# Performance work log

Hardware: AMD Instinct MI355X
Metric: run time of the kernel (lower is better)

Reference implementation:

```python
import jax, jax.numpy as jnp
import numpy as np

B, S, D, H = 2, 2048, 1024, 16
HD = D // H  # head dim 64
LN_EPS = 1e-12


def setup_inputs() -> dict:
    key = jax.random.key(0)
    ks = jax.random.split(key, 10)
    sc = 0.02
    return {
        "input_tensor": jax.random.normal(ks[0], (B, S, D), dtype=jnp.float32),
        "attention_mask": jnp.zeros((B, 1, 1, S), dtype=jnp.float32),
        "Wq": jax.random.normal(ks[1], (D, D), dtype=jnp.float32) * sc,
        "bq": jnp.zeros((D,), dtype=jnp.float32),
        "Wk": jax.random.normal(ks[2], (D, D), dtype=jnp.float32) * sc,
        "bk": jnp.zeros((D,), dtype=jnp.float32),
        "Wv": jax.random.normal(ks[3], (D, D), dtype=jnp.float32) * sc,
        "bv": jnp.zeros((D,), dtype=jnp.float32),
        "Wo": jax.random.normal(ks[4], (D, D), dtype=jnp.float32) * sc,
        "bo": jnp.zeros((D,), dtype=jnp.float32),
        "ln_gamma": jnp.ones((D,), dtype=jnp.float32),
        "ln_beta": jnp.zeros((D,), dtype=jnp.float32),
    }


def _split_heads(x):
    # [B,S,D] -> [B,H,S,hd]
    return x.reshape(B, S, H, HD).transpose(0, 2, 1, 3)


def reference(input_tensor, attention_mask, Wq, bq, Wk, bk, Wv, bv, Wo, bo, ln_gamma, ln_beta):
    q = _split_heads(input_tensor @ Wq + bq)
    k = _split_heads(input_tensor @ Wk + bk)
    v = _split_heads(input_tensor @ Wv + bv)
    scores = jnp.einsum("bhqd,bhkd->bhqk", q, k) / jnp.sqrt(jnp.float32(HD))
    scores = scores + attention_mask  # additive mask broadcast
    probs = jax.nn.softmax(scores, axis=-1)
    ctx = jnp.einsum("bhqk,bhkd->bhqd", probs, v)
    ctx = ctx.transpose(0, 2, 1, 3).reshape(B, S, D)
    hidden = ctx @ Wo + bo
    x = hidden + input_tensor
    mu = jnp.mean(x, axis=-1, keepdims=True)
    var = jnp.mean(jnp.square(x - mu), axis=-1, keepdims=True)
    return (x - mu) / jnp.sqrt(var + LN_EPS) * ln_gamma + ln_beta
```

## Files before the change

kernel.cpp:

```cpp
#include <hip/hip_runtime.h>
#include <stdint.h>

#define Bb 2
#define Ss 2048
#define Dd 1024
#define Hh 16
#define HD 64
#define Mtot 4096

typedef __bf16 bf16x8 __attribute__((ext_vector_type(8)));
typedef float f32x4 __attribute__((ext_vector_type(4)));
typedef unsigned short ushort_t;

#if __has_builtin(__builtin_amdgcn_exp2f)
#define EXP2(x) __builtin_amdgcn_exp2f(x)
#else
#define EXP2(x) __expf((x) * 0.6931472f)
#endif

__device__ __forceinline__ float bf2f(ushort_t u) {
    union { uint32_t i; float f; } v;
    v.i = ((uint32_t)u) << 16;
    return v.f;
}

__device__ __forceinline__ ushort_t f2bf(float f) {
    union { float f; uint32_t i; } v;
    v.f = f;
    uint32_t u = v.i;
    u += 0x7FFFu + ((u >> 16) & 1u);
    return (ushort_t)(u >> 16);
}

__device__ __forceinline__ uint32_t fbits(float f) {
    union { float f; uint32_t i; } v; v.f = f; return v.i;
}

__device__ __forceinline__ float load_in(const void* p, size_t i, int isf32) {
    if (isf32) return ((const float*)p)[i];
    return bf2f(((const ushort_t*)p)[i]);
}

__device__ __forceinline__ void gload_lds16(const void* g, void* l) {
    __builtin_amdgcn_global_load_lds(
        (const __attribute__((address_space(1))) void*)g,
        (__attribute__((address_space(3))) void*)l, 16, 0, 0);
}

#define NCONV 4204544ull
__global__ __launch_bounds__(256) void prep_k(
    const void* X, const void* mask, const void* bq, const void* bk,
    const void* bv, const void* bo, const void* g, const void* be,
    const void* Wq, const void* Wk, const void* Wv, const void* Wo,
    int* __restrict__ flag, ushort_t* __restrict__ cX,
    ushort_t* __restrict__ cMask, ushort_t* __restrict__ cB,
    ushort_t* __restrict__ wt) {
    __shared__ int sflag;
    __shared__ ushort_t tile[32][33];
    const int tid = threadIdx.x;
    {
        const int lane = tid & 63;
        if (tid < 64) {
            const ushort_t* Xu = (const ushort_t*)X;
            int local = 0;
            for (int i = lane; i < 2048; i += 64) {
                int e = (Xu[i] >> 7) & 0xFF;
                local += (e >= 0x90);
            }
            for (int off = 1; off < 64; off <<= 1) local += __shfl_xor(local, off);
            if (lane == 0) sflag = (local >= 4) ? 1 : 0;
        }
    }
    __syncthreads();
    const int f = sflag;
    if (blockIdx.x == 0 && tid == 0) *flag = f;

    if (blockIdx.x < 1024) {
        const size_t stride = 1024ull * 256ull;
        for (size_t i = (size_t)blockIdx.x * 256 + tid; i < NCONV; i += stride) {
            if (i < 4194304ull) {
                cX[i] = f2bf(load_in(X, i, f));
            } else if (i < 4198400ull) {
                size_t j = i - 4194304ull;
                cMask[j] = f2bf(load_in(mask, j, f));
            } else {
                size_t j = i - 4198400ull;
                int w = (int)(j >> 10);
                size_t r = j & 1023ull;
                const void* p = (w == 0) ? bq : (w == 1) ? bk : (w == 2) ? bv
                              : (w == 3) ? bo : (w == 4) ? g : be;
                cB[w * 1024 + r] = f2bf(load_in(p, r, f));
            }
        }
    } else {
        int id2 = blockIdx.x - 1024;
        int z = id2 >> 10;
        int rem = id2 & 1023;
        int bx = rem & 31, by = rem >> 5;
        const void* W = (z == 0) ? Wq : (z == 1) ? Wk : (z == 2) ? Wv : Wo;
        ushort_t* T = wt + (size_t)z * Dd * Dd;
        int tx = tid & 31, ty = tid >> 5;
        int x = bx * 32 + tx;
        int y0 = by * 32;
        for (int i = 0; i < 4; i++) {
            int y = y0 + ty + i * 8;
            tile[ty + i * 8][tx] = f2bf(load_in(W, (size_t)y * Dd + x, f));
        }
        __syncthreads();
        int x2 = by * 32 + tx;
        int y20 = bx * 32;
        for (int i = 0; i < 4; i++) {
            int y = y20 + ty + i * 8;
            T[(size_t)y * Dd + x2] = tile[tx][ty + i * 8];
        }
    }
}

__global__ __launch_bounds__(256) void gemm_qkv(
    const ushort_t* __restrict__ X, const ushort_t* __restrict__ wt,
    const ushort_t* __restrict__ cB,
    ushort_t* __restrict__ Qb, ushort_t* __restrict__ Kb, ushort_t* __restrict__ Vtb) {
    const int z = blockIdx.z;
    const ushort_t* Wt = wt + (size_t)z * Dd * Dd;
    const ushort_t* bias = cB + z * 1024;

    __shared__ __align__(16) ushort_t smem[2][2][128 * 32];

    const int tid = threadIdx.x;
    const int lane = tid & 63, wv = tid >> 6;
    const int quad = lane >> 4, l15 = lane & 15;
    const int wrow = (wv >> 1) * 64, wcol = (wv & 1) * 64;
    const int row0 = blockIdx.y * 128, col0 = blockIdx.x * 128;
    const int lrow = lane >> 2, lcol = (lane & 3) * 8;

    const f32x4 fzero = {0.f, 0.f, 0.f, 0.f};
    f32x4 acc[4][4];
    for (int mt = 0; mt < 4; mt++)
        for (int nt = 0; nt < 4; nt++) acc[mt][nt] = fzero;

    for (int j = 0; j < 2; j++) {
        int ch = wv * 2 + j;
        gload_lds16(&X[(size_t)(row0 + ch * 16 + lrow) * Dd + lcol],
                    &smem[0][0][ch * 512]);
        gload_lds16(&Wt[(size_t)(col0 + ch * 16 + lrow) * Dd + lcol],
                    &smem[0][1][ch * 512]);
    }

    for (int k0 = 0; k0 < Dd; k0 += 32) {
        const int buf = (k0 >> 5) & 1;
        __syncthreads();
        if (k0 + 32 < Dd) {
            for (int j = 0; j < 2; j++) {
                int ch = wv * 2 + j;
                gload_lds16(&X[(size_t)(row0 + ch * 16 + lrow) * Dd + k0 + 32 + lcol],
                            &smem[buf ^ 1][0][ch * 512]);
                gload_lds16(&Wt[(size_t)(col0 + ch * 16 + lrow) * Dd + k0 + 32 + lcol],
                            &smem[buf ^ 1][1][ch * 512]);
            }
        }
        const ushort_t* As = &smem[buf][0][0];
        const ushort_t* Bs = &smem[buf][1][0];
        bf16x8 af[4], bfr[4];
        for (int mt = 0; mt < 4; mt++)
            af[mt] = *(const bf16x8*)(&As[(wrow + mt * 16 + l15) * 32 + quad * 8]);
        for (int nt = 0; nt < 4; nt++)
            bfr[nt] = *(const bf16x8*)(&Bs[(wcol + nt * 16 + l15) * 32 + quad * 8]);
        for (int mt = 0; mt < 4; mt++)
            for (int nt = 0; nt < 4; nt++)
                acc[mt][nt] = __builtin_amdgcn_mfma_f32_16x16x32_bf16(
                    af[mt], bfr[nt], acc[mt][nt], 0, 0, 0);
    }

    const float qscale = 0.18033688f;
    ushort_t* Cs = &smem[0][0][0];
    for (int mt = 0; mt < 4; mt++) {
        __syncthreads();
        for (int nt = 0; nt < 4; nt++) {
            int gn = col0 + wcol + nt * 16 + l15;
            float bv_ = bf2f(bias[gn]);
            for (int r = 0; r < 4; r++) {
                float v = acc[mt][nt][r] + bv_;
                if (z == 0) v *= qscale;
                int ric = (wv >> 1) * 16 + quad * 4 + r;
                Cs[ric * 136 + wcol + nt * 16 + l15] = f2bf(v);
            }
        }
        __syncthreads();
        if (z == 2) {
            int c = tid >> 1, r0 = (tid & 1) * 16;
            int gn = col0 + c, h = gn >> 6, d = gn & 63;
            int gmbase = row0 + (r0 >> 4) * 64 + mt * 16;
            int b = gmbase >> 11, s0 = gmbase & 2047;
            union { ushort_t u[16]; uint4 q[2]; } pk;
            for (int i = 0; i < 16; i++) pk.u[i] = Cs[(r0 + i) * 136 + c];
            uint4* dst = (uint4*)&Vtb[((size_t)((b * Hh + h) * HD + d)) * Ss + s0];
            dst[0] = pk.q[0];
            dst[1] = pk.q[1];
        } else {
            int ric = tid >> 3, c0 = (tid & 7) * 16;
            int gm = row0 + (ric >> 4) * 64 + mt * 16 + (ric & 15);
            int gn = col0 + c0, h = gn >> 6, d0 = gn & 63;
            int b = gm >> 11, s = gm & 2047;
            const uint4* src = (const uint4*)&Cs[ric * 136 + c0];
            ushort_t* Ob = (z == 0) ? Qb : Kb;
            uint4* dst = (uint4*)&Ob[((size_t)((b * Hh + h) * Ss + s)) * HD + d0];
            dst[0] = src[0];
            dst[1] = src[1];
        }
    }
}

#define STR 36
__global__ __launch_bounds__(512) void attn(
    const ushort_t* __restrict__ Q, const ushort_t* __restrict__ K,
    const ushort_t* __restrict__ Vt, const ushort_t* __restrict__ mask,
    ushort_t* __restrict__ ctx) {
    const int tid = threadIdx.x;
    const int lane = tid & 63, wv = tid >> 6;
    const int quad = lane >> 4, l15 = lane & 15;
    const int bh = blockIdx.x;
    const int b = bh >> 4, h = bh & 15;
    const int q0 = blockIdx.y * 128 + wv * 16;

    const ushort_t* Qh = Q + (size_t)bh * Ss * HD;
    const ushort_t* Kh = K + (size_t)bh * Ss * HD;
    const ushort_t* Vh = Vt + (size_t)bh * HD * Ss;

    __shared__ __align__(16) ushort_t Ks[2][64 * 64];
    __shared__ __align__(16) ushort_t Vs[2][64 * 64];
    __shared__ __align__(16) float maskF[Ss];
    __shared__ __align__(16) ushort_t Pl[8][16 * STR];
    ushort_t* Pw = &Pl[wv][0];

    for (int i = tid; i < Ss; i += 512)
        maskF[i] = (bf2f(mask[b * Ss + i]) - 4.0f) * 1.4426950f;

    const int r8 = lane >> 3, c8 = lane & 7, gc = c8 ^ r8;
    const int sw = l15 & 7;

    gload_lds16(&Kh[(size_t)(wv * 8 + r8) * HD + gc * 8], &Ks[0][wv * 512]);
    gload_lds16(&Vh[(size_t)(wv * 8 + r8) * Ss + gc * 8], &Vs[0][wv * 512]);

    bf16x8 qf[2];
    qf[0] = *(const bf16x8*)(&Qh[(size_t)(q0 + l15) * HD + quad * 8]);
    qf[1] = *(const bf16x8*)(&Qh[(size_t)(q0 + l15) * HD + 32 + quad * 8]);

    bf16x8 onesf;
    {
        union { ushort_t u[8]; bf16x8 v; } ou;
        for (int i = 0; i < 8; i++) ou.u[i] = 0x3F80;
        onesf = ou.v;
    }

    const f32x4 fzero = {0.f, 0.f, 0.f, 0.f};
    f32x4 o[4];
    for (int dt = 0; dt < 4; dt++) o[dt] = fzero;
    f32x4 o_l = fzero;

    for (int kb = 0; kb < Ss; kb += 64) {
        const int buf = (kb >> 6) & 1;
        __syncthreads();

        if (kb + 64 < Ss) {
            gload_lds16(&Kh[(size_t)(kb + 64 + wv * 8 + r8) * HD + gc * 8],
                        &Ks[buf ^ 1][wv * 512]);
            gload_lds16(&Vh[(size_t)(wv * 8 + r8) * Ss + kb + 64 + gc * 8],
                        &Vs[buf ^ 1][wv * 512]);
        }

        const ushort_t* ks = &Ks[buf][0];
        const ushort_t* vs = &Vs[buf][0];

        f32x4 st[4];
        for (int kt = 0; kt < 4; kt++) {
            f32x4 mk = *(const f32x4*)(&maskF[kb + kt * 16 + quad * 4]);
            bf16x8 kf0 = *(const bf16x8*)(&ks[(kt * 16 + l15) * 64 + ((quad) ^ sw) * 8]);
            bf16x8 kf1 = *(const bf16x8*)(&ks[(kt * 16 + l15) * 64 + ((quad + 4) ^ sw) * 8]);
            st[kt] = __builtin_amdgcn_mfma_f32_16x16x32_bf16(kf0, qf[0], mk, 0, 0, 0);
            st[kt] = __builtin_amdgcn_mfma_f32_16x16x32_bf16(kf1, qf[1], st[kt], 0, 0, 0);
        }

        for (int kt = 0; kt < 4; kt++) {
            float e0 = EXP2(st[kt][0]);
            float e1 = EXP2(st[kt][1]);
            float e2 = EXP2(st[kt][2]);
            float e3 = EXP2(st[kt][3]);
            uint2 pk;
            pk.x = __builtin_amdgcn_perm(fbits(e1), fbits(e0), 0x07060302u);
            pk.y = __builtin_amdgcn_perm(fbits(e3), fbits(e2), 0x07060302u);
            *(uint2*)(&Pw[l15 * STR + kt * 16 + quad * 4]) = pk;
        }

        for (int c = 0; c < 2; c++) {
            union { uint2 u2[2]; bf16x8 v; } pu;
            pu.u2[0] = *(const uint2*)(&Pw[l15 * STR + c * 32 + quad * 8]);
            pu.u2[1] = *(const uint2*)(&Pw[l15 * STR + c * 32 + quad * 8 + 4]);
            bf16x8 pf = pu.v;
            for (int dt = 0; dt < 4; dt++) {
                bf16x8 vf = *(const bf16x8*)(
                    &vs[(dt * 16 + l15) * 64 + ((c * 4 + quad) ^ sw) * 8]);
                o[dt] = __builtin_amdgcn_mfma_f32_16x16x32_bf16(pf, vf, o[dt], 0, 0, 0);
            }
            o_l = __builtin_amdgcn_mfma_f32_16x16x32_bf16(pf, onesf, o_l, 0, 0, 0);
        }
    }

    for (int r = 0; r < 4; r++) {
        int q = q0 + quad * 4 + r;
        float linv = 1.f / o_l[r];
        for (int dt = 0; dt < 4; dt++) {
            ctx[((size_t)(b * Ss + q)) * Dd + h * HD + dt * 16 + l15] =
                f2bf(o[dt][r] * linv);
        }
    }
}

__global__ __launch_bounds__(256) void gemm_out(
    const ushort_t* __restrict__ A, const ushort_t* __restrict__ Wt,
    const ushort_t* __restrict__ bo, const ushort_t* __restrict__ X,
    ushort_t* __restrict__ xout) {
    __shared__ __align__(16) ushort_t smem[2][6144];

    const int tid = threadIdx.x;
    const int lane = tid & 63, wv = tid >> 6;
    const int quad = lane >> 4, l15 = lane & 15;
    const int wrow = (wv >> 1) * 32, wcol = (wv & 1) * 64;
    const int row0 = blockIdx.y * 64, col0 = blockIdx.x * 128;
    const int lrow = lane >> 2, lcol = (lane & 3) * 8;

    const f32x4 fzero = {0.f, 0.f, 0.f, 0.f};
    f32x4 acc[2][4];
    for (int mt = 0; mt < 2; mt++)
        for (int nt = 0; nt < 4; nt++) acc[mt][nt] = fzero;

    gload_lds16(&A[(size_t)(row0 + wv * 16 + lrow) * Dd + lcol], &smem[0][wv * 512]);
    for (int j = 0; j < 2; j++) {
        int ch = wv * 2 + j;
        gload_lds16(&Wt[(size_t)(col0 + ch * 16 + lrow) * Dd + lcol],
                    &smem[0][2048 + ch * 512]);
    }

    for (int k0 = 0; k0 < Dd; k0 += 32) {
        const int buf = (k0 >> 5) & 1;
        __syncthreads();
        if (k0 + 32 < Dd) {
            gload_lds16(&A[(size_t)(row0 + wv * 16 + lrow) * Dd + k0 + 32 + lcol],
                        &smem[buf ^ 1][wv * 512]);
            for (int j = 0; j < 2; j++) {
                int ch = wv * 2 + j;
                gload_lds16(&Wt[(size_t)(col0 + ch * 16 + lrow) * Dd + k0 + 32 + lcol],
                            &smem[buf ^ 1][2048 + ch * 512]);
            }
        }
        const ushort_t* As = &smem[buf][0];
        const ushort_t* Bs = &smem[buf][2048];
        bf16x8 af[2], bfr[4];
        for (int mt = 0; mt < 2; mt++)
            af[mt] = *(const bf16x8*)(&As[(wrow + mt * 16 + l15) * 32 + quad * 8]);
        for (int nt = 0; nt < 4; nt++)
            bfr[nt] = *(const bf16x8*)(&Bs[(wcol + nt * 16 + l15) * 32 + quad * 8]);
        for (int mt = 0; mt < 2; mt++)
            for (int nt = 0; nt < 4; nt++)
                acc[mt][nt] = __builtin_amdgcn_mfma_f32_16x16x32_bf16(
                    af[mt], bfr[nt], acc[mt][nt], 0, 0, 0);
    }

    for (int mt = 0; mt < 2; mt++)
        for (int nt = 0; nt < 4; nt++)
            for (int r = 0; r < 4; r++) {
                int gm = row0 + wrow + mt * 16 + quad * 4 + r;
                int gn = col0 + wcol + nt * 16 + l15;
                float v = acc[mt][nt][r] + bf2f(bo[gn]) + bf2f(X[(size_t)gm * Dd + gn]);
                xout[(size_t)gm * Dd + gn] = f2bf(v);
            }
}

__global__ __launch_bounds__(256) void ln_k(
    const ushort_t* __restrict__ x, const ushort_t* __restrict__ gamma,
    const ushort_t* __restrict__ beta, const int* __restrict__ flag,
    void* __restrict__ out) {
    const int row = blockIdx.x;
    const int tid = threadIdx.x;
    const int f = *flag;

    union { uint2 q; ushort_t u[4]; } xv;
    xv.q = ((const uint2*)(x + (size_t)row * Dd))[tid];
    float xi[4];
    for (int i = 0; i < 4; i++) xi[i] = bf2f(xv.u[i]);
    float s = (xi[0] + xi[1]) + (xi[2] + xi[3]);
    float ss = (xi[0] * xi[0] + xi[1] * xi[1]) + (xi[2] * xi[2] + xi[3] * xi[3]);
    for (int off = 1; off < 64; off <<= 1) {
        s += __shfl_xor(s, off);
        ss += __shfl_xor(ss, off);
    }
    __shared__ float ps[4], pss[4];
    int wv = tid >> 6;
    if ((tid & 63) == 0) { ps[wv] = s; pss[wv] = ss; }
    __syncthreads();
    s = ps[0] + ps[1] + ps[2] + ps[3];
    ss = pss[0] + pss[1] + pss[2] + pss[3];
    float mu = s * (1.f / Dd);
    float var = ss * (1.f / Dd) - mu * mu;
    float rstd = rsqrtf(fmaxf(var, 0.f) + 1e-12f);

    const int c0 = tid * 4;
    float r[4];
    for (int i = 0; i < 4; i++) {
        float g = bf2f(gamma[c0 + i]);
        float bb = bf2f(beta[c0 + i]);
        r[i] = (xi[i] - mu) * rstd * g + bb;
    }
    if (f) {
        float4 o4 = {r[0], r[1], r[2], r[3]};
        ((float4*)out)[(size_t)row * 256 + tid] = o4;
    } else {
        union { ushort_t u[4]; uint2 q; } pk;
        for (int i = 0; i < 4; i++) pk.u[i] = f2bf(r[i]);
        *(uint2*)((ushort_t*)out + (size_t)row * Dd + c0) = pk.q;
    }
}

extern "C" void kernel_launch(void* const* d_in, const int* in_sizes, int n_in,
                              void* d_out, int out_size, void* d_ws, size_t ws_size,
                              hipStream_t stream) {
    char* ws = (char*)d_ws;
    int* flag       = (int*)ws;
    ushort_t* cMask = (ushort_t*)(ws + (64ull << 10));
    ushort_t* cB    = (ushort_t*)(ws + (96ull << 10));
    ushort_t* cX    = (ushort_t*)(ws + (1ull << 20));
    ushort_t* wt    = (ushort_t*)(ws + (17ull << 20));
    ushort_t* Qb    = (ushort_t*)(ws + (25ull << 20));
    ushort_t* Kb    = (ushort_t*)(ws + (33ull << 20));
    ushort_t* Vtb   = (ushort_t*)(ws + (41ull << 20));
    ushort_t* ctx   = (ushort_t*)(ws + (49ull << 20));
    ushort_t* xbuf  = (ushort_t*)(ws + (25ull << 20));

    hipLaunchKernelGGL(prep_k, dim3(5120), dim3(256), 0, stream,
                       d_in[0], d_in[1], d_in[3], d_in[5], d_in[7], d_in[9],
                       d_in[10], d_in[11], d_in[2], d_in[4], d_in[6], d_in[8],
                       flag, cX, cMask, cB, wt);
    hipLaunchKernelGGL(gemm_qkv, dim3(8, 32, 3), dim3(256), 0, stream,
                       cX, wt, cB, Qb, Kb, Vtb);
    hipLaunchKernelGGL(attn, dim3(32, 16), dim3(512), 0, stream,
                       Qb, Kb, Vtb, cMask, ctx);
    hipLaunchKernelGGL(gemm_out, dim3(8, 64), dim3(256), 0, stream,
                       ctx, wt + 3ull * Dd * Dd, cB + 3 * 1024, cX, xbuf);
    hipLaunchKernelGGL(ln_k, dim3(Mtot), dim3(256), 0, stream,
                       xbuf, cB + 4 * 1024, cB + 5 * 1024, flag, d_out);
}
```

Before: 210.5 us.

## Vectorize input conversion, write Q/K epilogue directly, widen attention LDS stride

The prep kernel now converts inputs eight elements at a time with float4 loads and uint4 stores, and copies directly when the input is already bf16. The Q/K projection epilogue drops the shared-memory staging and its barriers, writing scalar bf16 values straight to global memory. The V path keeps the LDS transpose. The attention kernel's LDS padding stride constant changes from 36 to 76, which alters the bank-conflict pattern and LDS footprint. Direct scalar stores can give less coalesced 2-byte writes than the previous 16-byte stores.

```diff
diff --git a/kernel.cpp b/kernel.cpp
--- a/kernel.cpp
+++ b/kernel.cpp
@@ -47,7 +47,7 @@
         (__attribute__((address_space(3))) void*)l, 16, 0, 0);
 }
 
-#define NCONV 4204544ull
+#define NVEC 525568ull
 __global__ __launch_bounds__(256) void prep_k(
     const void* X, const void* mask, const void* bq, const void* bk,
     const void* bv, const void* bo, const void* g, const void* be,
@@ -77,19 +77,33 @@
 
     if (blockIdx.x < 1024) {
         const size_t stride = 1024ull * 256ull;
-        for (size_t i = (size_t)blockIdx.x * 256 + tid; i < NCONV; i += stride) {
-            if (i < 4194304ull) {
-                cX[i] = f2bf(load_in(X, i, f));
-            } else if (i < 4198400ull) {
-                size_t j = i - 4194304ull;
-                cMask[j] = f2bf(load_in(mask, j, f));
+        for (size_t t = (size_t)blockIdx.x * 256 + tid; t < NVEC; t += stride) {
+            const void* src;
+            ushort_t* dst;
+            size_t v;
+            if (t < 524288ull) {
+                src = X; dst = cX; v = t;
+            } else if (t < 524800ull) {
+                src = mask; dst = cMask; v = t - 524288ull;
             } else {
-                size_t j = i - 4198400ull;
-                int w = (int)(j >> 10);
-                size_t r = j & 1023ull;
-                const void* p = (w == 0) ? bq : (w == 1) ? bk : (w == 2) ? bv
-                              : (w == 3) ? bo : (w == 4) ? g : be;
-                cB[w * 1024 + r] = f2bf(load_in(p, r, f));
+                size_t j = t - 524800ull;
+                int w = (int)(j >> 7);
+                src = (w == 0) ? bq : (w == 1) ? bk : (w == 2) ? bv
+                    : (w == 3) ? bo : (w == 4) ? g : be;
+                dst = cB + w * 1024;
+                v = j & 127;
+            }
+            if (f) {
+                const float4* s4 = (const float4*)src;
+                float4 a = s4[v * 2], b = s4[v * 2 + 1];
+                union { ushort_t u[8]; uint4 q; } pk;
+                pk.u[0] = f2bf(a.x); pk.u[1] = f2bf(a.y);
+                pk.u[2] = f2bf(a.z); pk.u[3] = f2bf(a.w);
+                pk.u[4] = f2bf(b.x); pk.u[5] = f2bf(b.y);
+                pk.u[6] = f2bf(b.z); pk.u[7] = f2bf(b.w);
+                ((uint4*)dst)[v] = pk.q;
+            } else {
+                ((uint4*)dst)[v] = ((const uint4*)src)[v];
             }
         }
     } else {
@@ -172,21 +186,35 @@
     }
 
     const float qscale = 0.18033688f;
-    ushort_t* Cs = &smem[0][0][0];
-    for (int mt = 0; mt < 4; mt++) {
-        __syncthreads();
-        for (int nt = 0; nt < 4; nt++) {
-            int gn = col0 + wcol + nt * 16 + l15;
-            float bv_ = bf2f(bias[gn]);
-            for (int r = 0; r < 4; r++) {
-                float v = acc[mt][nt][r] + bv_;
-                if (z == 0) v *= qscale;
-                int ric = (wv >> 1) * 16 + quad * 4 + r;
-                Cs[ric * 136 + wcol + nt * 16 + l15] = f2bf(v);
-            }
-        }
-        __syncthreads();
-        if (z == 2) {
+    if (z != 2) {
+        ushort_t* Ob = (z == 0) ? Qb : Kb;
+        for (int mt = 0; mt < 4; mt++)
+            for (int nt = 0; nt < 4; nt++) {
+                int gn = col0 + wcol + nt * 16 + l15;
+                int h = gn >> 6, d = gn & 63;
+                float bv_ = bf2f(bias[gn]);
+                for (int r = 0; r < 4; r++) {
+                    int gm = row0 + wrow + mt * 16 + quad * 4 + r;
+                    float v = acc[mt][nt][r] + bv_;
+                    if (z == 0) v *= qscale;
+                    int b = gm >> 11, s = gm & 2047;
+                    Ob[((size_t)((b * Hh + h) * Ss + s)) * HD + d] = f2bf(v);
+                }
+            }
+    } else {
+        ushort_t* Cs = &smem[0][0][0];
+        for (int mt = 0; mt < 4; mt++) {
+            __syncthreads();
+            for (int nt = 0; nt < 4; nt++) {
+                int gn = col0 + wcol + nt * 16 + l15;
+                float bv_ = bf2f(bias[gn]);
+                for (int r = 0; r < 4; r++) {
+                    float v = acc[mt][nt][r] + bv_;
+                    int ric = (wv >> 1) * 16 + quad * 4 + r;
+                    Cs[ric * 136 + wcol + nt * 16 + l15] = f2bf(v);
+                }
+            }
+            __syncthreads();
             int c = tid >> 1, r0 = (tid & 1) * 16;
             int gn = col0 + c, h = gn >> 6, d = gn & 63;
             int gmbase = row0 + (r0 >> 4) * 64 + mt * 16;
@@ -196,21 +224,11 @@
             uint4* dst = (uint4*)&Vtb[((size_t)((b * Hh + h) * HD + d)) * Ss + s0];
             dst[0] = pk.q[0];
             dst[1] = pk.q[1];
-        } else {
-            int ric = tid >> 3, c0 = (tid & 7) * 16;
-            int gm = row0 + (ric >> 4) * 64 + mt * 16 + (ric & 15);
-            int gn = col0 + c0, h = gn >> 6, d0 = gn & 63;
-            int b = gm >> 11, s = gm & 2047;
-            const uint4* src = (const uint4*)&Cs[ric * 136 + c0];
-            ushort_t* Ob = (z == 0) ? Qb : Kb;
-            uint4* dst = (uint4*)&Ob[((size_t)((b * Hh + h) * Ss + s)) * HD + d0];
-            dst[0] = src[0];
-            dst[1] = src[1];
-        }
-    }
-}
-
-#define STR 36
+        }
+    }
+}
+
+#define STR 76
 __global__ __launch_bounds__(512) void attn(
     const ushort_t* __restrict__ Q, const ushort_t* __restrict__ K,
     const ushort_t* __restrict__ Vt, const ushort_t* __restrict__ mask,
```

New measurement: 216.6 us. +2.9%, slower.
